# Kernel optimization log

Measured on AMD Instinct MI355X. Metric: run time of the kernel, lower is better.

## Reference

```python
import jax, jax.numpy as jnp
import numpy as np

V, E, H = 32000, 512, 1024
B, T = 32, 48
PAD = 0


def setup_inputs() -> dict:
    key = jax.random.key(0)
    ks = jax.random.split(key, 9)
    s = 0.05
    emb = jax.random.normal(ks[0], (V, E), jnp.float32) * s
    emb = emb.at[PAD].set(0.0)  # padding_idx row is zero in nn.Embedding
    return {
        "initial_hidden_state": jax.random.normal(ks[1], (B, H), jnp.float32),
        "target_sequence": jax.random.randint(ks[2], (B, T), 0, V),
        "emb": emb,
        "W_ih": jax.random.normal(ks[3], (3 * H, E), jnp.float32) * s,  # [r;z;n] input weights
        "W_hh": jax.random.normal(ks[4], (3 * H, H), jnp.float32) * s,
        "b_ih": jax.random.normal(ks[5], (3 * H,), jnp.float32) * s,
        "b_hh": jax.random.normal(ks[6], (3 * H,), jnp.float32) * s,
        "W_cls": jax.random.normal(ks[7], (V, H), jnp.float32) * s,
        "b_cls": jax.random.normal(ks[8], (V,), jnp.float32) * s,
    }


def _decode(initial_hidden_state, target_sequence, emb, W_ih, W_hh, b_ih, b_hh, W_cls, b_cls):
    # teacher forcing: sample_probability = 0.0 -> use_sample False
    idx_t = target_sequence.T  # [T, B]

    def step(h, y_idx):
        x = emb[y_idx]                                 # [B, E] embedding gather
        gi = x @ W_ih.T + b_ih                         # [B, 3H]
        gh = h @ W_hh.T + b_hh                         # [B, 3H]
        i_r, i_z, i_n = jnp.split(gi, 3, axis=-1)
        h_r, h_z, h_n = jnp.split(gh, 3, axis=-1)
        r = jax.nn.sigmoid(i_r + h_r)
        z = jax.nn.sigmoid(i_z + h_z)
        n = jnp.tanh(i_n + r * h_n)
        h_new = (1.0 - z) * n + z * h                  # torch GRUCell update
        score = h_new @ W_cls.T + b_cls                # [B, V]
        return h_new, score

    _, scores = jax.lax.scan(step, initial_hidden_state, idx_t)  # [T, B, V]
    return jnp.transpose(scores, (1, 0, 2))                      # [B, T, V]


def reference(initial_hidden_state, target_sequence, emb, W_ih, W_hh, b_ih, b_hh, W_cls, b_cls):
    return _decode(initial_hidden_state, target_sequence, emb, W_ih, W_hh, b_ih, b_hh, W_cls, b_cls)
```

## Files before the change

### kernel.cpp

```cpp
#include <hip/hip_runtime.h>
#include <hip/hip_bf16.h>

typedef __attribute__((ext_vector_type(8))) short short8;
typedef __attribute__((ext_vector_type(4))) float f32x4;
typedef __attribute__((ext_vector_type(4))) unsigned int u32x4;

#define T_STEPS 48
#define BATCH 32
#define EDIM 512
#define HDIM 1024
#define VOCAB 32000
#define GRU_BLOCKS 64
#define JPB 16
#define SENT 0x7FFF7FFFu
#define N_BIG 625
#define N_TILES 875
#define CNT_STRIDE 16
#define EARLY_WORKERS 96

#define HS_T_STRIDE 16384

__device__ __forceinline__ unsigned short f2bf(float f) {
    __hip_bfloat16 h = __float2bfloat16(f);
    return *reinterpret_cast<unsigned short*>(&h);
}
__device__ __forceinline__ float bf2f(unsigned short u) {
    union { unsigned int i; float f; } v;
    v.i = ((unsigned int)u) << 16;
    return v.f;
}

typedef __attribute__((address_space(1))) const void GAS;
typedef __attribute__((address_space(3))) void LAS;
__device__ __forceinline__ void gload_lds16(const unsigned short* g, unsigned short* l) {
    __builtin_amdgcn_global_load_lds((GAS*)g, (LAS*)(unsigned)(uintptr_t)l, 16, 0, 0);
}

__device__ __forceinline__ void store16_coh(unsigned int* p, u32x4 v) {
    asm volatile("global_store_dwordx4 %0, %1, off sc0 sc1"
                 :: "v"((unsigned long long)(uintptr_t)p), "v"(v) : "memory");
}

__global__ __launch_bounds__(256) void prep_kernel(
    const float* __restrict__ h0, const int* __restrict__ tseq,
    const float* __restrict__ emb, const float* __restrict__ w_ih,
    const float* __restrict__ w_hh, const float* __restrict__ w_cls,
    unsigned short* __restrict__ wcls_bf, unsigned short* __restrict__ wih_bf,
    unsigned short* __restrict__ whh_bf, unsigned short* __restrict__ x_bf,
    unsigned int* __restrict__ hs32, unsigned int* __restrict__ cnt8)
{
    const long R0 = (long)VOCAB * HDIM / 4;
    const long R1 = (long)3 * HDIM * EDIM / 4;
    const long R2 = (long)3 * HDIM * HDIM / 4;
    const long R3 = (long)T_STEPS * BATCH * EDIM / 4;
    const long R4 = (long)HS_T_STRIDE;
    const long R5 = (long)T_STEPS * HS_T_STRIDE / 4;
    const long R6 = 512;
    const long total = R0 + R1 + R2 + R3 + R4 + R5 + R6;

    for (long i = (long)blockIdx.x * blockDim.x + threadIdx.x; i < total;
         i += (long)gridDim.x * blockDim.x) {
        if (i < R0) {
            float4 v = reinterpret_cast<const float4*>(w_cls)[i];
            ushort4 u = { f2bf(v.x), f2bf(v.y), f2bf(v.z), f2bf(v.w) };
            *reinterpret_cast<ushort4*>(wcls_bf + i * 4) = u;
        } else if (i < R0 + R1) {
            long j = i - R0;
            float4 v = reinterpret_cast<const float4*>(w_ih)[j];
            ushort4 u = { f2bf(v.x), f2bf(v.y), f2bf(v.z), f2bf(v.w) };
            *reinterpret_cast<ushort4*>(wih_bf + j * 4) = u;
        } else if (i < R0 + R1 + R2) {
            long j = i - R0 - R1;
            float4 v = reinterpret_cast<const float4*>(w_hh)[j];
            ushort4 u = { f2bf(v.x), f2bf(v.y), f2bf(v.z), f2bf(v.w) };
            *reinterpret_cast<ushort4*>(whh_bf + j * 4) = u;
        } else if (i < R0 + R1 + R2 + R3) {
            long j = i - R0 - R1 - R2;
            int m = (int)(j >> 7);
            int kk4 = (int)(j & 127);
            int t = m >> 5, b = m & 31;
            int tok = tseq[b * T_STEPS + t];
            float4 v = reinterpret_cast<const float4*>(emb)[(long)tok * (EDIM / 4) + kk4];
            ushort4 u = { f2bf(v.x), f2bf(v.y), f2bf(v.z), f2bf(v.w) };
            *reinterpret_cast<ushort4*>(x_bf + (long)m * EDIM + kk4 * 4) = u;
        } else if (i < R0 + R1 + R2 + R3 + R4) {
            long j = i - R0 - R1 - R2 - R3;
            int w = (int)(j >> 5), b = (int)(j & 31);
            unsigned short a = f2bf(h0[b * HDIM + 2 * w]);
            unsigned short c = f2bf(h0[b * HDIM + 2 * w + 1]);
            hs32[j] = (unsigned)a | ((unsigned)c << 16);
        } else if (i < R0 + R1 + R2 + R3 + R4 + R5) {
            long j = i - R0 - R1 - R2 - R3 - R4;
            uint4 s = { SENT, SENT, SENT, SENT };
            reinterpret_cast<uint4*>(hs32 + HS_T_STRIDE)[j] = s;
        } else {
            long j = i - R0 - R1 - R2 - R3 - R4 - R5;
            uint4 z = { 0u, 0u, 0u, 0u };
            reinterpret_cast<uint4*>(cnt8)[j] = z;
        }
    }
}

__global__ __launch_bounds__(256) void gemm_gi(
    const unsigned short* __restrict__ A, const unsigned short* __restrict__ B,
    const float* __restrict__ bias, float* __restrict__ C, int K, int Ntot, int nM)
{
    const int nwg = gridDim.x;
    const int lin = blockIdx.x;
    const int q = nwg >> 3;
    const int wg = (lin & 7) * q + (lin >> 3);
    const int mi = wg % nM, ni = wg / nM;
    const int m0 = mi * 128, n0 = ni * 128;

    const int tid = threadIdx.x;
    const int lane = tid & 63;
    const int wid = tid >> 6;
    const int wr = wid >> 1, wc = wid & 1;

    __shared__ __align__(16) unsigned short As[128 * 32];
    __shared__ __align__(16) unsigned short Bs[128 * 32];

    f32x4 acc[4][4] = {};
    const int NT = K >> 5;
    const int srow = (lane >> 2);
    const int skk = (lane & 3) * 8;

    for (int kt = 0; kt < NT; ++kt) {
        __syncthreads();
        {
            const int kb = kt * 32;
#pragma unroll
            for (int h2 = 0; h2 < 2; ++h2) {
                const int i = wid + h2 * 4;
                const int row = i * 16 + srow;
                gload_lds16(A + (size_t)(m0 + row) * K + kb + skk, As + i * 512);
                gload_lds16(B + (size_t)(n0 + row) * K + kb + skk, Bs + i * 512);
            }
        }
        __syncthreads();

        const int kg = lane >> 4;
        const int l15 = lane & 15;
        short8 af[4], bf[4];
#pragma unroll
        for (int i = 0; i < 4; ++i) {
            af[i] = *(const short8*)(As + ((wr * 64 + i * 16 + l15) * 32 + kg * 8));
            bf[i] = *(const short8*)(Bs + ((wc * 64 + i * 16 + l15) * 32 + kg * 8));
        }
#pragma unroll
        for (int i = 0; i < 4; ++i)
#pragma unroll
            for (int j = 0; j < 4; ++j)
                acc[i][j] = __builtin_amdgcn_mfma_f32_16x16x32_bf16(af[i], bf[j], acc[i][j], 0, 0, 0);
    }

    const int l15 = lane & 15, lhi = lane >> 4;
#pragma unroll
    for (int i = 0; i < 4; ++i)
#pragma unroll
        for (int j = 0; j < 4; ++j) {
            int col = n0 + wc * 64 + j * 16 + l15;
            float bv = bias[col];
#pragma unroll
            for (int q2 = 0; q2 < 4; ++q2) {
                int row = m0 + wr * 64 + i * 16 + lhi * 4 + q2;
                C[(size_t)row * Ntot + col] = acc[i][j][q2] + bv;
            }
        }
}

__global__ __launch_bounds__(512, 1) void fused_kernel(
    unsigned int* __restrict__ hs32, unsigned int* __restrict__ hrow32,
    const unsigned short* __restrict__ whh_bf,
    const float* __restrict__ gi, const float* __restrict__ b_hh,
    const float* __restrict__ h0,
    const unsigned short* __restrict__ wcls_bf, const float* __restrict__ b_cls,
    float* __restrict__ out, unsigned int* __restrict__ cnt8,
    unsigned int* __restrict__ tileq)
{
    __shared__ __align__(16) char smem[124160];
    __shared__ unsigned short Hs[BATCH][JPB];
    __shared__ int sTile;

    const int tid = threadIdx.x;
    const int bid = blockIdx.x;
    const int lane = tid & 63, wid = tid >> 6;
    const int l15 = lane & 15, kg = lane >> 4;

    if (bid < GRU_BLOCKS) {
        unsigned short (*Wl)[1032] = reinterpret_cast<unsigned short (*)[1032]>(smem);
        float (*P)[32][49] = reinterpret_cast<float (*)[32][49]>(smem + 99072);

        const int j0 = bid * JPB;
        for (int c = tid; c < 48 * 128; c += 512) {
            int row = c >> 7, k8 = (c & 127) * 8;
            int g = row >> 4, jj = row & 15;
            *(short8*)&Wl[row][k8] =
                *(const short8*)(whh_bf + (size_t)(g * HDIM + j0 + jj) * HDIM + k8);
        }
        const int b = tid >> 4, jj = tid & 15;
        const int gj = j0 + jj;
        const float bhr = b_hh[gj];
        const float bhz = b_hh[HDIM + gj];
        const float bhn = b_hh[2 * HDIM + gj];
        float hloc = h0[b * HDIM + gj];
        __syncthreads();

        for (int t = 0; t < T_STEPS; ++t) {
            const size_t tb = (size_t)t * HS_T_STRIDE;
            const float* gr = gi + (size_t)(t * BATCH + b) * (3 * HDIM);
            float xr = gr[gj], xz = gr[HDIM + gj], xn = gr[2 * HDIM + gj];

            if (tid < 256) {
                if (t) {
                    const unsigned int* cp = cnt8 + (size_t)t * CNT_STRIDE + 2 * wid;
                    for (;;) {
                        unsigned ok = (lane < 2)
                            ? (__hip_atomic_load(cp + lane, __ATOMIC_RELAXED, __HIP_MEMORY_SCOPE_AGENT) >= 8u ? 1u : 0u)
                            : 1u;
                        if (__all(ok != 0u)) break;
                        __builtin_amdgcn_s_sleep(2);
                    }
                    asm volatile("" ::: "memory");
                }

                const int kq = wid * 256;
                unsigned wv[8][8];
#pragma unroll
                for (int ks = 0; ks < 8; ++ks) {
                    const int wbase = wid * 128 + ks * 16 + kg * 4;
#pragma unroll
                    for (int mi2 = 0; mi2 < 2; ++mi2) {
                        const int bb = mi2 * 16 + l15;
#pragma unroll
                        for (int q = 0; q < 4; ++q)
                            wv[ks][mi2 * 4 + q] = *(const unsigned*)(
                                hs32 + tb + (size_t)(wbase + q) * 32 + bb);
                    }
                }
                for (;;) {
                    int bad = 0;
#pragma unroll
                    for (int ks = 0; ks < 8; ++ks)
#pragma unroll
                        for (int i = 0; i < 8; ++i)
                            bad |= (wv[ks][i] == SENT);
                    if (!__any(bad)) break;
                    __builtin_amdgcn_s_sleep(1);
#pragma unroll
                    for (int ks = 0; ks < 8; ++ks)
#pragma unroll
                        for (int i = 0; i < 8; ++i)
                            if (wv[ks][i] == SENT) {
                                const int mi2 = i >> 2, q = i & 3;
                                wv[ks][i] = __hip_atomic_load(
                                    hs32 + tb + (size_t)(wid * 128 + ks * 16 + kg * 4 + q) * 32 + (mi2 * 16 + l15),
                                    __ATOMIC_RELAXED, __HIP_MEMORY_SCOPE_AGENT);
                            }
                }
                f32x4 acc[2][3] = {};
#pragma unroll
                for (int ks = 0; ks < 8; ++ks) {
                    const int kb = kq + ks * 32 + kg * 8;
                    union U8 { unsigned u[4]; short8 s; };
                    short8 ah[2];
#pragma unroll
                    for (int mi2 = 0; mi2 < 2; ++mi2) {
                        U8 x;
#pragma unroll
                        for (int q = 0; q < 4; ++q) x.u[q] = wv[ks][mi2 * 4 + q];
                        ah[mi2] = x.s;
                    }
#pragma unroll
                    for (int fr = 0; fr < 3; ++fr) {
                        short8 bh = *(const short8*)&Wl[fr * 16 + l15][kb];
#pragma unroll
                        for (int mi2 = 0; mi2 < 2; ++mi2)
                            acc[mi2][fr] = __builtin_amdgcn_mfma_f32_16x16x32_bf16(ah[mi2], bh, acc[mi2][fr], 0, 0, 0);
                    }
                }
#pragma unroll
                for (int mi2 = 0; mi2 < 2; ++mi2)
#pragma unroll
                    for (int fr = 0; fr < 3; ++fr)
#pragma unroll
                        for (int q = 0; q < 4; ++q)
                            P[wid][mi2 * 16 + kg * 4 + q][fr * 16 + l15] = acc[mi2][fr][q];
            }
            __syncthreads();

            {
                float ghr = 0.f, ghz = 0.f, ghn = 0.f;
#pragma unroll
                for (int w = 0; w < 4; ++w) {
                    ghr += P[w][b][jj];
                    ghz += P[w][b][16 + jj];
                    ghn += P[w][b][32 + jj];
                }
                float r = 1.f / (1.f + __expf(-(xr + ghr + bhr)));
                float z = 1.f / (1.f + __expf(-(xz + ghz + bhz)));
                float n = tanhf(xn + r * (ghn + bhn));
                float hnew = (1.f - z) * n + z * hloc;
                hloc = hnew;
                Hs[b][jj] = f2bf(hnew);
            }
            __syncthreads();

            if (tid < 64) {
                const int q = tid >> 3, c = tid & 7;
                u32x4 d;
#pragma unroll
                for (int w2 = 0; w2 < 4; ++w2) {
                    int bb = c * 4 + w2;
                    d[w2] = (unsigned)Hs[bb][2 * q] | ((unsigned)Hs[bb][2 * q + 1] << 16);
                }
                store16_coh(hs32 + (size_t)(t + 1) * HS_T_STRIDE + (size_t)((j0 >> 1) + q) * 32 + c * 4, d);
            } else if (tid < 128) {
                const int i = tid - 64, bb = i >> 1, half = i & 1;
                u32x4 d;
#pragma unroll
                for (int w2 = 0; w2 < 4; ++w2) {
                    int q = half * 4 + w2;
                    d[w2] = (unsigned)Hs[bb][2 * q] | ((unsigned)Hs[bb][2 * q + 1] << 16);
                }
                store16_coh(hrow32 + ((size_t)t * BATCH + bb) * 512 + (j0 >> 1) + half * 4, d);
            }
            __syncthreads();
            if (tid == 0)
                __hip_atomic_fetch_add(cnt8 + (size_t)(t + 1) * CNT_STRIDE + (bid >> 3), 1u,
                                       __ATOMIC_RELAXED, __HIP_MEMORY_SCOPE_AGENT);
        }
    } else if (bid >= GRU_BLOCKS + EARLY_WORKERS) {
        if (wid == 0) {
            const unsigned int* cp = cnt8 + (size_t)T_STEPS * CNT_STRIDE;
            for (;;) {
                unsigned v = (lane < 8)
                    ? __hip_atomic_load(cp + lane, __ATOMIC_RELAXED, __HIP_MEMORY_SCOPE_AGENT)
                    : 8u;
                if (__all(v >= 8u)) break;
                __builtin_amdgcn_s_sleep(64);
            }
        }
        __syncthreads();
    }

    const unsigned short* hrowA = (const unsigned short*)hrow32;
    const int srow = lane >> 2;
    const int skk = (lane & 3) * 8;

    for (;;) {
        __syncthreads();
        if (tid == 0)
            sTile = (int)__hip_atomic_fetch_add(tileq, 1u, __ATOMIC_RELAXED, __HIP_MEMORY_SCOPE_AGENT);
        __syncthreads();
        const int k = sTile;
        if (k >= N_TILES) break;

        int mi, m0, n0, big;
        if (k < N_BIG) { mi = k / 125; n0 = (k - mi * 125) * 256; m0 = mi * 256; big = 1; }
        else { int idx = k - N_BIG; mi = 5; m0 = 1280 + (idx & 1) * 128; n0 = (idx >> 1) * 256; big = 0; }

        {
            if (wid == 0) {
                const unsigned int* cp = cnt8 + (size_t)(mi * 8 + 8) * CNT_STRIDE;
                for (;;) {
                    unsigned v = (lane < 8)
                        ? __hip_atomic_load(cp + lane, __ATOMIC_RELAXED, __HIP_MEMORY_SCOPE_AGENT)
                        : 8u;
                    if (__all(v >= 8u)) break;
                    __builtin_amdgcn_s_sleep(32);
                }
            }
            __syncthreads();
            asm volatile("" ::: "memory");
        }

        if (big) {
            const int wm = wid >> 1, wn = wid & 1;
            unsigned short* As0 = (unsigned short*)(smem);
            unsigned short* Bs0 = (unsigned short*)(smem + 16384);
            unsigned short* As1 = (unsigned short*)(smem + 32768);
            unsigned short* Bs1 = (unsigned short*)(smem + 49152);
            f32x4 acc[4][8] = {};

#define STAGE(KT, AB, BB)                                                      \
            {                                                                  \
                const int kb = (KT) * 32;                                      \
                _Pragma("unroll")                                              \
                for (int h2 = 0; h2 < 2; ++h2) {                               \
                    const int i = wid + h2 * 8;                                \
                    const int row = i * 16 + srow;                             \
                    gload_lds16(hrowA + (size_t)(m0 + row) * HDIM + kb + skk, (AB) + i * 512); \
                    gload_lds16(wcls_bf + (size_t)(n0 + row) * HDIM + kb + skk, (BB) + i * 512); \
                }                                                              \
            }
#define COMPUTE(AB, BB)                                                        \
            {                                                                  \
                short8 af[4], bf[8];                                           \
                _Pragma("unroll")                                              \
                for (int i = 0; i < 4; ++i)                                    \
                    af[i] = *(const short8*)((AB) + ((wm * 64 + i * 16 + l15) * 32 + kg * 8)); \
                _Pragma("unroll")                                              \
                for (int j = 0; j < 8; ++j)                                    \
                    bf[j] = *(const short8*)((BB) + ((wn * 128 + j * 16 + l15) * 32 + kg * 8)); \
                _Pragma("unroll")                                              \
                for (int i = 0; i < 4; ++i)                                    \
                    _Pragma("unroll")                                          \
                    for (int j = 0; j < 8; ++j)                                \
                        acc[i][j] = __builtin_amdgcn_mfma_f32_16x16x32_bf16(af[i], bf[j], acc[i][j], 0, 0, 0); \
            }
            STAGE(0, As0, Bs0);
            __syncthreads();
            for (int it = 0; it < 16; ++it) {
                const int kt0 = 2 * it;
                STAGE(kt0 + 1, As1, Bs1);
                COMPUTE(As0, Bs0);
                __syncthreads();
                if (kt0 + 2 < 32) STAGE(kt0 + 2, As0, Bs0);
                COMPUTE(As1, Bs1);
                __syncthreads();
            }
#undef STAGE
#undef COMPUTE
            const int lhi = lane >> 4;
#pragma unroll
            for (int i = 0; i < 4; ++i)
#pragma unroll
                for (int j = 0; j < 8; ++j) {
                    int col = n0 + wn * 128 + j * 16 + l15;
                    float bv = b_cls[col];
#pragma unroll
                    for (int q2 = 0; q2 < 4; ++q2) {
                        int row = m0 + wm * 64 + i * 16 + lhi * 4 + q2;
                        int t = row >> 5, bb = row & 31;
                        __builtin_nontemporal_store(acc[i][j][q2] + bv,
                            &out[(size_t)(bb * T_STEPS + t) * VOCAB + col]);
                    }
                }
        } else {
            const int wm = wid >> 2, wn = wid & 3;
            unsigned short* As0 = (unsigned short*)(smem);
            unsigned short* Bs0 = (unsigned short*)(smem + 8192);
            unsigned short* As1 = (unsigned short*)(smem + 24576);
            unsigned short* Bs1 = (unsigned short*)(smem + 32768);
            f32x4 acc[4][4] = {};

#define STAGE1(KT, AB, BB)                                                     \
            {                                                                  \
                const int kb = (KT) * 32;                                      \
                _Pragma("unroll")                                              \
                for (int h2 = 0; h2 < 3; ++h2) {                               \
                    const int c = wid * 3 + h2;                     \
                    if (c < 8) {                                               \
                        const int row = c * 16 + srow;                         \
                        gload_lds16(hrowA + (size_t)(m0 + row) * HDIM + kb + skk, (AB) + c * 512); \
                    } else {                                                   \
                        const int row = (c - 8) * 16 + srow;                   \
                        gload_lds16(wcls_bf + (size_t)(n0 + row) * HDIM + kb + skk, (BB) + (c - 8) * 512); \
                    }                                                          \
                }                                                              \
            }
#define COMPUTE1(AB, BB)                                                       \
            {                                                                  \
                short8 af[4], bf[4];                                           \
                _Pragma("unroll")                                              \
                for (int i = 0; i < 4; ++i)                                    \
                    af[i] = *(const short8*)((AB) + ((wm * 64 + i * 16 + l15) * 32 + kg * 8)); \
                _Pragma("unroll")                                              \
                for (int j = 0; j < 4; ++j)                                    \
                    bf[j] = *(const short8*)((BB) + ((wn * 64 + j * 16 + l15) * 32 + kg * 8)); \
                _Pragma("unroll")                                              \
                for (int i = 0; i < 4; ++i)                                    \
                    _Pragma("unroll")                                          \
                    for (int j = 0; j < 4; ++j)                                \
                        acc[i][j] = __builtin_amdgcn_mfma_f32_16x16x32_bf16(af[i], bf[j], acc[i][j], 0, 0, 0); \
            }
            STAGE1(0, As0, Bs0);
            __syncthreads();
            for (int it = 0; it < 16; ++it) {
                const int kt0 = 2 * it;
                STAGE1(kt0 + 1, As1, Bs1);
                COMPUTE1(As0, Bs0);
                __syncthreads();
                if (kt0 + 2 < 32) STAGE1(kt0 + 2, As0, Bs0);
                COMPUTE1(As1, Bs1);
                __syncthreads();
            }
#undef STAGE1
#undef COMPUTE1
            const int lhi = lane >> 4;
#pragma unroll
            for (int i = 0; i < 4; ++i)
#pragma unroll
                for (int j = 0; j < 4; ++j) {
                    int col = n0 + wn * 64 + j * 16 + l15;
                    float bv = b_cls[col];
#pragma unroll
                    for (int q2 = 0; q2 < 4; ++q2) {
                        int row = m0 + wm * 64 + i * 16 + lhi * 4 + q2;
                        int t = row >> 5, bb = row & 31;
                        __builtin_nontemporal_store(acc[i][j][q2] + bv,
                            &out[(size_t)(bb * T_STEPS + t) * VOCAB + col]);
                    }
                }
        }
    }
}

extern "C" void kernel_launch(void* const* d_in, const int* in_sizes, int n_in,
                              void* d_out, int out_size, void* d_ws, size_t ws_size,
                              hipStream_t stream) {
    const float* h0    = (const float*)d_in[0];
    const int*   tseq  = (const int*)d_in[1];
    const float* emb   = (const float*)d_in[2];
    const float* w_ih  = (const float*)d_in[3];
    const float* w_hh  = (const float*)d_in[4];
    const float* b_ih  = (const float*)d_in[5];
    const float* b_hh  = (const float*)d_in[6];
    const float* w_cls = (const float*)d_in[7];
    const float* b_cls = (const float*)d_in[8];
    float* out = (float*)d_out;

    char* w = (char*)d_ws;
    unsigned short* wcls_bf = (unsigned short*)w; w += (size_t)VOCAB * HDIM * 2;
    unsigned short* wih_bf  = (unsigned short*)w; w += (size_t)3 * HDIM * EDIM * 2;
    unsigned short* whh_bf  = (unsigned short*)w; w += (size_t)3 * HDIM * HDIM * 2;
    unsigned short* x_bf    = (unsigned short*)w; w += (size_t)T_STEPS * BATCH * EDIM * 2;
    unsigned int*   hs32    = (unsigned int*)w;   w += (size_t)(T_STEPS + 1) * HS_T_STRIDE * 4;
    unsigned int*   hrow32  = (unsigned int*)w;   w += (size_t)T_STEPS * BATCH * 512 * 4;
    float* gi               = (float*)w;          w += (size_t)T_STEPS * BATCH * 3 * HDIM * 4;
    unsigned int* cnt8      = (unsigned int*)w;   w += 8192;
    unsigned int* tileq     = cnt8 + 1024;

    prep_kernel<<<2048, 256, 0, stream>>>(h0, tseq, emb, w_ih, w_hh, w_cls,
                                          wcls_bf, wih_bf, whh_bf, x_bf, hs32, cnt8);

    gemm_gi<<<(T_STEPS * BATCH / 128) * (3 * HDIM / 128), 256, 0, stream>>>(
        x_bf, wih_bf, b_ih, gi, EDIM, 3 * HDIM, T_STEPS * BATCH / 128);

    fused_kernel<<<256, 512, 0, stream>>>(hs32, hrow32, whh_bf, gi, b_hh, h0,
                                          wcls_bf, b_cls, out, cnt8, tileq);
}
```

Baseline: 343.2 us.

## Overlap W_cls bf16 conversion with GRU recurrence inside fused kernel

Moves the large W_cls fp32-to-bf16 conversion out of the prep kernel into the 192 non-GRU blocks of the fused kernel, so it runs while the 64 GRU blocks do the serial recurrence. A global counter signals completion, and all blocks wait for it before starting classifier tiles. This takes the conversion off the critical path, but the GRU blocks and early workers now spin on that counter before tile work. It also depends on the counter slot being zeroed by prep, which appears to be the case since offset 1056 falls inside the 2048-word zeroed region.

```diff
diff --git a/kernel.cpp b/kernel.cpp
--- a/kernel.cpp
+++ b/kernel.cpp
@@ -44,38 +44,33 @@
 __global__ __launch_bounds__(256) void prep_kernel(
     const float* __restrict__ h0, const int* __restrict__ tseq,
     const float* __restrict__ emb, const float* __restrict__ w_ih,
-    const float* __restrict__ w_hh, const float* __restrict__ w_cls,
-    unsigned short* __restrict__ wcls_bf, unsigned short* __restrict__ wih_bf,
-    unsigned short* __restrict__ whh_bf, unsigned short* __restrict__ x_bf,
+    const float* __restrict__ w_hh,
+    unsigned short* __restrict__ wih_bf, unsigned short* __restrict__ whh_bf,
+    unsigned short* __restrict__ x_bf,
     unsigned int* __restrict__ hs32, unsigned int* __restrict__ cnt8)
 {
-    const long R0 = (long)VOCAB * HDIM / 4;
     const long R1 = (long)3 * HDIM * EDIM / 4;
     const long R2 = (long)3 * HDIM * HDIM / 4;
     const long R3 = (long)T_STEPS * BATCH * EDIM / 4;
     const long R4 = (long)HS_T_STRIDE;
     const long R5 = (long)T_STEPS * HS_T_STRIDE / 4;
     const long R6 = 512;
-    const long total = R0 + R1 + R2 + R3 + R4 + R5 + R6;
+    const long total = R1 + R2 + R3 + R4 + R5 + R6;
 
     for (long i = (long)blockIdx.x * blockDim.x + threadIdx.x; i < total;
          i += (long)gridDim.x * blockDim.x) {
-        if (i < R0) {
-            float4 v = reinterpret_cast<const float4*>(w_cls)[i];
-            ushort4 u = { f2bf(v.x), f2bf(v.y), f2bf(v.z), f2bf(v.w) };
-            *reinterpret_cast<ushort4*>(wcls_bf + i * 4) = u;
-        } else if (i < R0 + R1) {
-            long j = i - R0;
+        if (i < R1) {
+            long j = i;
             float4 v = reinterpret_cast<const float4*>(w_ih)[j];
             ushort4 u = { f2bf(v.x), f2bf(v.y), f2bf(v.z), f2bf(v.w) };
             *reinterpret_cast<ushort4*>(wih_bf + j * 4) = u;
-        } else if (i < R0 + R1 + R2) {
-            long j = i - R0 - R1;
+        } else if (i < R1 + R2) {
+            long j = i - R1;
             float4 v = reinterpret_cast<const float4*>(w_hh)[j];
             ushort4 u = { f2bf(v.x), f2bf(v.y), f2bf(v.z), f2bf(v.w) };
             *reinterpret_cast<ushort4*>(whh_bf + j * 4) = u;
-        } else if (i < R0 + R1 + R2 + R3) {
-            long j = i - R0 - R1 - R2;
+        } else if (i < R1 + R2 + R3) {
+            long j = i - R1 - R2;
             int m = (int)(j >> 7);
             int kk4 = (int)(j & 127);
             int t = m >> 5, b = m & 31;
@@ -83,18 +78,18 @@
             float4 v = reinterpret_cast<const float4*>(emb)[(long)tok * (EDIM / 4) + kk4];
             ushort4 u = { f2bf(v.x), f2bf(v.y), f2bf(v.z), f2bf(v.w) };
             *reinterpret_cast<ushort4*>(x_bf + (long)m * EDIM + kk4 * 4) = u;
-        } else if (i < R0 + R1 + R2 + R3 + R4) {
-            long j = i - R0 - R1 - R2 - R3;
+        } else if (i < R1 + R2 + R3 + R4) {
+            long j = i - R1 - R2 - R3;
             int w = (int)(j >> 5), b = (int)(j & 31);
             unsigned short a = f2bf(h0[b * HDIM + 2 * w]);
             unsigned short c = f2bf(h0[b * HDIM + 2 * w + 1]);
             hs32[j] = (unsigned)a | ((unsigned)c << 16);
-        } else if (i < R0 + R1 + R2 + R3 + R4 + R5) {
-            long j = i - R0 - R1 - R2 - R3 - R4;
+        } else if (i < R1 + R2 + R3 + R4 + R5) {
+            long j = i - R1 - R2 - R3 - R4;
             uint4 s = { SENT, SENT, SENT, SENT };
             reinterpret_cast<uint4*>(hs32 + HS_T_STRIDE)[j] = s;
         } else {
-            long j = i - R0 - R1 - R2 - R3 - R4 - R5;
+            long j = i - R1 - R2 - R3 - R4 - R5;
             uint4 z = { 0u, 0u, 0u, 0u };
             reinterpret_cast<uint4*>(cnt8)[j] = z;
         }
@@ -174,7 +169,8 @@
     const unsigned short* __restrict__ whh_bf,
     const float* __restrict__ gi, const float* __restrict__ b_hh,
     const float* __restrict__ h0,
-    const unsigned short* __restrict__ wcls_bf, const float* __restrict__ b_cls,
+    const float* __restrict__ wcls_f, unsigned short* __restrict__ wcls_bf,
+    const float* __restrict__ b_cls,
     float* __restrict__ out, unsigned int* __restrict__ cnt8,
     unsigned int* __restrict__ tileq)
 {
@@ -186,6 +182,8 @@
     const int bid = blockIdx.x;
     const int lane = tid & 63, wid = tid >> 6;
     const int l15 = lane & 15, kg = lane >> 4;
+
+    unsigned int* wcnt = cnt8 + 1056;
 
     if (bid < GRU_BLOCKS) {
         unsigned short (*Wl)[1032] = reinterpret_cast<unsigned short (*)[1032]>(smem);
@@ -330,19 +328,46 @@
                 __hip_atomic_fetch_add(cnt8 + (size_t)(t + 1) * CNT_STRIDE + (bid >> 3), 1u,
                                        __ATOMIC_RELAXED, __HIP_MEMORY_SCOPE_AGENT);
         }
-    } else if (bid >= GRU_BLOCKS + EARLY_WORKERS) {
-        if (wid == 0) {
-            const unsigned int* cp = cnt8 + (size_t)T_STEPS * CNT_STRIDE;
-            for (;;) {
-                unsigned v = (lane < 8)
-                    ? __hip_atomic_load(cp + lane, __ATOMIC_RELAXED, __HIP_MEMORY_SCOPE_AGENT)
-                    : 8u;
-                if (__all(v >= 8u)) break;
-                __builtin_amdgcn_s_sleep(64);
-            }
-        }
-        __syncthreads();
+    } else {
+        {
+            const long UNITS = (long)VOCAB * HDIM / 8;
+            unsigned int* dst = (unsigned int*)wcls_bf;
+            for (long u = (long)(bid - GRU_BLOCKS) * 512 + tid; u < UNITS; u += 192L * 512) {
+                const float* src = wcls_f + u * 8;
+                u32x4 d;
+#pragma unroll
+                for (int p = 0; p < 4; ++p) {
+                    unsigned lo = f2bf(src[2 * p]);
+                    unsigned hi = f2bf(src[2 * p + 1]);
+                    d[p] = lo | (hi << 16);
+                }
+                store16_coh(dst + u * 4, d);
+            }
+            __syncthreads();
+            if (tid == 0)
+                __hip_atomic_fetch_add(wcnt, 1u, __ATOMIC_RELAXED, __HIP_MEMORY_SCOPE_AGENT);
+        }
+        if (bid >= GRU_BLOCKS + EARLY_WORKERS) {
+            if (wid == 0) {
+                const unsigned int* cp = cnt8 + (size_t)T_STEPS * CNT_STRIDE;
+                for (;;) {
+                    unsigned v = (lane < 8)
+                        ? __hip_atomic_load(cp + lane, __ATOMIC_RELAXED, __HIP_MEMORY_SCOPE_AGENT)
+                        : 8u;
+                    if (__all(v >= 8u)) break;
+                    __builtin_amdgcn_s_sleep(64);
+                }
+            }
+            __syncthreads();
+        }
     }
+
+    if (tid == 0) {
+        while (__hip_atomic_load(wcnt, __ATOMIC_RELAXED, __HIP_MEMORY_SCOPE_AGENT) < 192u)
+            __builtin_amdgcn_s_sleep(16);
+    }
+    __syncthreads();
+    asm volatile("" ::: "memory");
 
     const unsigned short* hrowA = (const unsigned short*)hrow32;
     const int srow = lane >> 2;
@@ -532,12 +557,12 @@
     unsigned int* cnt8      = (unsigned int*)w;   w += 8192;
     unsigned int* tileq     = cnt8 + 1024;
 
-    prep_kernel<<<2048, 256, 0, stream>>>(h0, tseq, emb, w_ih, w_hh, w_cls,
-                                          wcls_bf, wih_bf, whh_bf, x_bf, hs32, cnt8);
+    prep_kernel<<<2048, 256, 0, stream>>>(h0, tseq, emb, w_ih, w_hh,
+                                          wih_bf, whh_bf, x_bf, hs32, cnt8);
 
     gemm_gi<<<(T_STEPS * BATCH / 128) * (3 * HDIM / 128), 256, 0, stream>>>(
         x_bf, wih_bf, b_ih, gi, EDIM, 3 * HDIM, T_STEPS * BATCH / 128);
 
     fused_kernel<<<256, 512, 0, stream>>>(hs32, hrow32, whh_bf, gi, b_hh, h0,
-                                          wcls_bf, b_cls, out, cnt8, tileq);
-}
+                                          w_cls, wcls_bf, b_cls, out, cnt8, tileq);
+}
```

After: 330.8 us. 3.6% less time.
